# Kernel tuning notes

Measured on AMD Instinct MI355X. Metric: run time of the kernel, lower is better.

## Reference

```python
import jax, jax.numpy as jnp
import numpy as np

N = 16777216  # length of the returns series


def setup_inputs() -> dict:
    key = jax.random.key(0)
    returns = 0.01 * jax.random.normal(key, (N,), dtype=jnp.float32)
    return {
        "returns": returns,
        "omega": jnp.float32(0.01),
        "alpha": jnp.float32(0.1),
        "beta": jnp.float32(0.85),
    }


def reference(returns, omega, alpha, beta):
    # GARCH(1,1): h[0] = var(returns) (unbiased, matching torch.var default);
    # h[t] = omega + alpha * r[t-1]^2 + beta * h[t-1]
    h0 = jnp.var(returns, ddof=1)
    # drivers b_t = omega + alpha * r_{t-1}^2 for t = 1..n-1
    b = omega + alpha * jnp.square(returns[:-1])

    def step(h_prev, b_t):
        h_t = b_t + beta * h_prev
        return h_t, h_t

    _, h_rest = jax.lax.scan(step, h0, b)
    h = jnp.concatenate([h0[None], h_rest])  # [n]
    return jnp.sqrt(h), h
```

## Files before the change

### kernel.cpp

```cpp
#include <hip/hip_runtime.h>
#include <math.h>


#define KPW 2048
#define MAIN_BLOCK 256
#define FIX 256

typedef float v4f __attribute__((ext_vector_type(4)));

__global__ __launch_bounds__(MAIN_BLOCK, 8)
void garch_fused(const float* __restrict__ r, int n,
                 const float* __restrict__ pOmega, const float* __restrict__ pAlpha,
                 const float* __restrict__ pBeta,
                 float* __restrict__ out_sqrt, float* __restrict__ out_h,
                 double* __restrict__ partial) {
    const int lane = threadIdx.x & 63;
    const int wid  = threadIdx.x >> 6;
    const int gwave = (blockIdx.x * blockDim.x + threadIdx.x) >> 6;
    const int start = gwave * KPW;

    const float omega = *pOmega;
    const float alpha = *pAlpha;
    const float beta  = *pBeta;

    const float c1 = beta;
    const float c2 = c1 * c1;
    const float c3 = c2 * c1;
    const float c4 = c2 * c2;
    const float c8 = c4 * c4;
    const float c16 = c8 * c8;
    const float c32 = c16 * c16;
    const float c64 = c32 * c32;
    const float c128 = c64 * c64;

    double acc_s = 0.0, acc_q = 0.0;

    if (start + KPW <= n) {
        float pw1 = 1.0f;
        { float p = c1; int e = lane;
          if (e & 1)  pw1 *= p; p *= p;
          if (e & 2)  pw1 *= p; p *= p;
          if (e & 4)  pw1 *= p; p *= p;
          if (e & 8)  pw1 *= p; p *= p;
          if (e & 16) pw1 *= p; p *= p;
          if (e & 32) pw1 *= p; }
        float pw4 = 1.0f;
        { float p = c4; int e = lane;
          if (e & 1)  pw4 *= p; p *= p;
          if (e & 2)  pw4 *= p; p *= p;
          if (e & 4)  pw4 *= p; p *= p;
          if (e & 8)  pw4 *= p; p *= p;
          if (e & 16) pw4 *= p; p *= p;
          if (e & 32) pw4 *= p; }

        const float4* r4p = (const float4*)r;
        const int b4 = (start >> 2) + lane;

        float4 rv[8];
        #pragma unroll
        for (int k = 0; k < 8; ++k) rv[k] = r4p[b4 + 64 * k];

        float h_prev = 0.0f;
        float carry_r = 0.0f;
        if (start > 0) {
            float ra = r[start - 2 - lane];
            float rb = r[start - 66 - lane];
            carry_r  = r[start - 1];
            float ba = fmaf(alpha * ra, ra, omega);
            float bb = fmaf(alpha * rb, rb, omega);
            float part = pw1 * fmaf(c64, bb, ba);
            for (int d = 1; d < 64; d <<= 1) part += __shfl_xor(part, d, 64);
            h_prev = part;
        }

        #pragma unroll
        for (int k = 0; k < 8; k += 2) {
            float4 a = rv[k], b = rv[k + 1];
            float sf = ((a.x + a.y) + (a.z + a.w)) + ((b.x + b.y) + (b.z + b.w));
            float qf = fmaf(a.x, a.x, fmaf(a.y, a.y, fmaf(a.z, a.z, a.w * a.w)));
            qf = fmaf(b.x, b.x, fmaf(b.y, b.y, fmaf(b.z, b.z, fmaf(b.w, b.w, qf))));
            acc_s += (double)sf;
            acc_q += (double)qf;
        }

        #pragma unroll
        for (int k = 0; k < 8; ++k) {
            float4 v = rv[k];

            float prevw = __shfl_up(v.w, 1, 64);
            float segc  = (k == 0) ? carry_r : __shfl(rv[k - 1].w, 63, 64);
            float prev  = (lane == 0) ? segc : prevw;

            float b0 = fmaf(alpha * prev, prev, omega);
            float b1 = fmaf(alpha * v.x, v.x, omega);
            float b2 = fmaf(alpha * v.y, v.y, omega);
            float b3 = fmaf(alpha * v.z, v.z, omega);
            if (k == 0 && start == 0 && lane == 0) b0 = 0.0f;

            float B = fmaf(c1, b2, b3);
            B = fmaf(c2, b1, B);
            B = fmaf(c3, b0, B);

            float t;
            t = __shfl_up(B, 1, 64);  if (lane >= 1)  B = fmaf(c4,   t, B);
            t = __shfl_up(B, 2, 64);  if (lane >= 2)  B = fmaf(c8,   t, B);
            t = __shfl_up(B, 4, 64);  if (lane >= 4)  B = fmaf(c16,  t, B);
            t = __shfl_up(B, 8, 64);  if (lane >= 8)  B = fmaf(c32,  t, B);
            t = __shfl_up(B, 16, 64); if (lane >= 16) B = fmaf(c64,  t, B);
            t = __shfl_up(B, 32, 64); if (lane >= 32) B = fmaf(c128, t, B);

            float Bex = __shfl_up(B, 1, 64);
            if (lane == 0) Bex = 0.0f;
            float hb = fmaf(pw4, h_prev, Bex);

            float h0v = fmaf(c1, hb,  b0);
            float h1v = fmaf(c1, h0v, b1);
            float h2v = fmaf(c1, h1v, b2);
            float h3v = fmaf(c1, h2v, b3);

            v4f hs = {h0v, h1v, h2v, h3v};
            v4f sq = {sqrtf(h0v), sqrtf(h1v), sqrtf(h2v), sqrtf(h3v)};
            ((v4f*)out_h)[b4 + 64 * k]    = hs;
            ((v4f*)out_sqrt)[b4 + 64 * k] = sq;

            h_prev = __shfl(h3v, 63, 64);
        }
    } else if (start < n) {
        float h_prev = 0.0f;
        if (start > 0) {
            float pw1 = 1.0f;
            { float p = c1; int e = lane;
              if (e & 1)  pw1 *= p; p *= p;
              if (e & 2)  pw1 *= p; p *= p;
              if (e & 4)  pw1 *= p; p *= p;
              if (e & 8)  pw1 *= p; p *= p;
              if (e & 16) pw1 *= p; p *= p;
              if (e & 32) pw1 *= p; }
            float ra = r[start - 2 - lane];
            float rb = r[start - 66 - lane];
            float ba = fmaf(alpha * ra, ra, omega);
            float bb = fmaf(alpha * rb, rb, omega);
            float part = pw1 * fmaf(c64, bb, ba);
            for (int d = 1; d < 64; d <<= 1) part += __shfl_xor(part, d, 64);
            h_prev = part;
        }
        if (lane == 0) {
            float h = h_prev;
            float prevr = (start > 0) ? r[start - 1] : 0.0f;
            for (int tt = start; tt < n; ++tt) {
                float bb = fmaf(alpha * prevr, prevr, omega);
                if (tt == 0) bb = 0.0f;
                float hv = fmaf(beta, h, bb);
                out_sqrt[tt] = sqrtf(hv);
                out_h[tt] = hv;
                h = hv;
                prevr = r[tt];
                acc_s += (double)prevr;
                acc_q += (double)prevr * prevr;
            }
        }
    }

    for (int d = 1; d < 64; d <<= 1) {
        acc_s += __shfl_xor(acc_s, d, 64);
        acc_q += __shfl_xor(acc_q, d, 64);
    }
    __shared__ double ls[MAIN_BLOCK / 64], lq[MAIN_BLOCK / 64];
    if (lane == 0) { ls[wid] = acc_s; lq[wid] = acc_q; }
    __syncthreads();
    if (threadIdx.x == 0) {
        double S = 0.0, Q = 0.0;
        for (int w = 0; w < (int)(blockDim.x >> 6); ++w) { S += ls[w]; Q += lq[w]; }
        partial[2 * blockIdx.x]     = S;
        partial[2 * blockIdx.x + 1] = Q;
    }
}

__global__ void garch_finalize(const double* __restrict__ partial, int nblocks, int n,
                               const float* __restrict__ r,
                               const float* __restrict__ pOmega,
                               const float* __restrict__ pAlpha,
                               const float* __restrict__ pBeta,
                               float* __restrict__ out_sqrt, float* __restrict__ out_h) {
    __shared__ float rbuf[FIX];
    int fix = (n < FIX) ? n : FIX;
    for (int i = threadIdx.x; i < fix - 1; i += blockDim.x) rbuf[i] = r[i];

    double s = 0.0, q = 0.0;
    for (int i = threadIdx.x; i < nblocks; i += blockDim.x) {
        s += partial[2 * i];
        q += partial[2 * i + 1];
    }
    for (int d = 1; d < 64; d <<= 1) {
        s += __shfl_xor(s, d, 64);
        q += __shfl_xor(q, d, 64);
    }
    __shared__ double ls[4], lq[4];
    int wid = threadIdx.x >> 6, lane = threadIdx.x & 63;
    if (lane == 0) { ls[wid] = s; lq[wid] = q; }
    __syncthreads();
    if (threadIdx.x == 0) {
        double S = 0.0, Q = 0.0;
        for (int w = 0; w < (int)(blockDim.x >> 6); ++w) { S += ls[w]; Q += lq[w]; }
        double mean = S / (double)n;
        double var = (Q - (double)n * mean * mean) / (double)(n - 1);
        float h0 = (float)var;
        float omega = *pOmega, alpha = *pAlpha, beta = *pBeta;

        float h = h0;
        if (n > 0) { out_h[0] = h; out_sqrt[0] = sqrtf(h); }
        for (int t = 1; t < fix; ++t) {
            float rr = rbuf[t - 1];
            float b = fmaf(alpha * rr, rr, omega);
            h = fmaf(beta, h, b);
            out_h[t] = h;
            out_sqrt[t] = sqrtf(h);
        }
    }
}

extern "C" void kernel_launch(void* const* d_in, const int* in_sizes, int n_in,
                              void* d_out, int out_size, void* d_ws, size_t ws_size,
                              hipStream_t stream) {
    const float* r      = (const float*)d_in[0];
    const float* pOmega = (const float*)d_in[1];
    const float* pAlpha = (const float*)d_in[2];
    const float* pBeta  = (const float*)d_in[3];
    int n = in_sizes[0];

    float* out_sqrt = (float*)d_out;
    float* out_h    = out_sqrt + n;

    double* partial = (double*)d_ws;

    int elems_per_block = KPW * (MAIN_BLOCK / 64);
    int nblocks = (n + elems_per_block - 1) / elems_per_block;

    garch_fused<<<nblocks, MAIN_BLOCK, 0, stream>>>(
        r, n, pOmega, pAlpha, pBeta, out_sqrt, out_h, partial);
    garch_finalize<<<1, 256, 0, stream>>>(
        partial, nblocks, n, r, pOmega, pAlpha, pBeta, out_sqrt, out_h);
}
```

Before: 228.9 us.

## Double per-wave chunk and stream loads in a rolled loop instead of preloading

Each wave now processes 4096 elements instead of 2048, which halves the number of waves and the per-wave warm-up cost of the 128-element carry-in reduction. The 8-deep float4 preload with a fully unrolled scan is replaced by a rolled loop that loads one float4 per lane per 256-element step. A tail path handles partial chunks. The occupancy hint in launch bounds is dropped. In exchange, fewer loads are in flight per wave, each load now sits on the serial chain before its scan, and the grid has fewer blocks, so latency hiding may get worse.

```diff
diff --git a/kernel.cpp b/kernel.cpp
--- a/kernel.cpp
+++ b/kernel.cpp
@@ -2,13 +2,13 @@
 #include <math.h>
 
 
-#define KPW 2048
+#define KPW 4096
 #define MAIN_BLOCK 256
 #define FIX 256
 
 typedef float v4f __attribute__((ext_vector_type(4)));
 
-__global__ __launch_bounds__(MAIN_BLOCK, 8)
+__global__ __launch_bounds__(MAIN_BLOCK)
 void garch_fused(const float* __restrict__ r, int n,
                  const float* __restrict__ pOmega, const float* __restrict__ pAlpha,
                  const float* __restrict__ pBeta,
@@ -35,9 +35,9 @@
 
     double acc_s = 0.0, acc_q = 0.0;
 
-    if (start + KPW <= n) {
+    if (start < n) {
         float pw1 = 1.0f;
-        { float p = c1; int e = lane;
+        { float p = beta; int e = lane;
           if (e & 1)  pw1 *= p; p *= p;
           if (e & 2)  pw1 *= p; p *= p;
           if (e & 4)  pw1 *= p; p *= p;
@@ -53,89 +53,11 @@
           if (e & 16) pw4 *= p; p *= p;
           if (e & 32) pw4 *= p; }
 
-        const float4* r4p = (const float4*)r;
-        const int b4 = (start >> 2) + lane;
-
-        float4 rv[8];
-        #pragma unroll
-        for (int k = 0; k < 8; ++k) rv[k] = r4p[b4 + 64 * k];
-
-        float h_prev = 0.0f;
-        float carry_r = 0.0f;
-        if (start > 0) {
-            float ra = r[start - 2 - lane];
-            float rb = r[start - 66 - lane];
-            carry_r  = r[start - 1];
-            float ba = fmaf(alpha * ra, ra, omega);
-            float bb = fmaf(alpha * rb, rb, omega);
-            float part = pw1 * fmaf(c64, bb, ba);
-            for (int d = 1; d < 64; d <<= 1) part += __shfl_xor(part, d, 64);
-            h_prev = part;
-        }
-
-        #pragma unroll
-        for (int k = 0; k < 8; k += 2) {
-            float4 a = rv[k], b = rv[k + 1];
-            float sf = ((a.x + a.y) + (a.z + a.w)) + ((b.x + b.y) + (b.z + b.w));
-            float qf = fmaf(a.x, a.x, fmaf(a.y, a.y, fmaf(a.z, a.z, a.w * a.w)));
-            qf = fmaf(b.x, b.x, fmaf(b.y, b.y, fmaf(b.z, b.z, fmaf(b.w, b.w, qf))));
-            acc_s += (double)sf;
-            acc_q += (double)qf;
-        }
-
-        #pragma unroll
-        for (int k = 0; k < 8; ++k) {
-            float4 v = rv[k];
-
-            float prevw = __shfl_up(v.w, 1, 64);
-            float segc  = (k == 0) ? carry_r : __shfl(rv[k - 1].w, 63, 64);
-            float prev  = (lane == 0) ? segc : prevw;
-
-            float b0 = fmaf(alpha * prev, prev, omega);
-            float b1 = fmaf(alpha * v.x, v.x, omega);
-            float b2 = fmaf(alpha * v.y, v.y, omega);
-            float b3 = fmaf(alpha * v.z, v.z, omega);
-            if (k == 0 && start == 0 && lane == 0) b0 = 0.0f;
-
-            float B = fmaf(c1, b2, b3);
-            B = fmaf(c2, b1, B);
-            B = fmaf(c3, b0, B);
-
-            float t;
-            t = __shfl_up(B, 1, 64);  if (lane >= 1)  B = fmaf(c4,   t, B);
-            t = __shfl_up(B, 2, 64);  if (lane >= 2)  B = fmaf(c8,   t, B);
-            t = __shfl_up(B, 4, 64);  if (lane >= 4)  B = fmaf(c16,  t, B);
-            t = __shfl_up(B, 8, 64);  if (lane >= 8)  B = fmaf(c32,  t, B);
-            t = __shfl_up(B, 16, 64); if (lane >= 16) B = fmaf(c64,  t, B);
-            t = __shfl_up(B, 32, 64); if (lane >= 32) B = fmaf(c128, t, B);
-
-            float Bex = __shfl_up(B, 1, 64);
-            if (lane == 0) Bex = 0.0f;
-            float hb = fmaf(pw4, h_prev, Bex);
-
-            float h0v = fmaf(c1, hb,  b0);
-            float h1v = fmaf(c1, h0v, b1);
-            float h2v = fmaf(c1, h1v, b2);
-            float h3v = fmaf(c1, h2v, b3);
-
-            v4f hs = {h0v, h1v, h2v, h3v};
-            v4f sq = {sqrtf(h0v), sqrtf(h1v), sqrtf(h2v), sqrtf(h3v)};
-            ((v4f*)out_h)[b4 + 64 * k]    = hs;
-            ((v4f*)out_sqrt)[b4 + 64 * k] = sq;
-
-            h_prev = __shfl(h3v, 63, 64);
-        }
-    } else if (start < n) {
-        float h_prev = 0.0f;
-        if (start > 0) {
-            float pw1 = 1.0f;
-            { float p = c1; int e = lane;
-              if (e & 1)  pw1 *= p; p *= p;
-              if (e & 2)  pw1 *= p; p *= p;
-              if (e & 4)  pw1 *= p; p *= p;
-              if (e & 8)  pw1 *= p; p *= p;
-              if (e & 16) pw1 *= p; p *= p;
-              if (e & 32) pw1 *= p; }
+        float h_prev, r_carry;
+        if (start == 0) {
+            h_prev = 0.0f;
+            r_carry = 0.0f;
+        } else {
             float ra = r[start - 2 - lane];
             float rb = r[start - 66 - lane];
             float ba = fmaf(alpha * ra, ra, omega);
@@ -143,11 +65,67 @@
             float part = pw1 * fmaf(c64, bb, ba);
             for (int d = 1; d < 64; d <<= 1) part += __shfl_xor(part, d, 64);
             h_prev = part;
-        }
-        if (lane == 0) {
+            r_carry = r[start - 1];
+        }
+
+        int end = start + KPW; if (end > n) end = n;
+        const float4* r4p = (const float4*)r;
+
+        int s = start;
+        for (; s + 256 <= end; s += 256) {
+            float4 rv = r4p[(s >> 2) + lane];
+
+            float sf = (rv.x + rv.y) + (rv.z + rv.w);
+            float qf = fmaf(rv.x, rv.x,
+                       fmaf(rv.y, rv.y,
+                       fmaf(rv.z, rv.z, rv.w * rv.w)));
+            acc_s += (double)sf;
+            acc_q += (double)qf;
+
+            float prev = __shfl_up(rv.w, 1, 64);
+            if (lane == 0) prev = r_carry;
+
+            float b0 = fmaf(alpha * prev, prev, omega);
+            float b1 = fmaf(alpha * rv.x, rv.x, omega);
+            float b2 = fmaf(alpha * rv.y, rv.y, omega);
+            float b3 = fmaf(alpha * rv.z, rv.z, omega);
+            if (s == 0 && lane == 0) b0 = 0.0f;
+
+            float B = fmaf(c1, b2, b3);
+            B = fmaf(c2, b1, B);
+            B = fmaf(c3, b0, B);
+
+            float t;
+            t = __shfl_up(B, 1, 64);  if (lane >= 1)  B = fmaf(c4,  t, B);
+            t = __shfl_up(B, 2, 64);  if (lane >= 2)  B = fmaf(c8,  t, B);
+            t = __shfl_up(B, 4, 64);  if (lane >= 4)  B = fmaf(c16, t, B);
+            t = __shfl_up(B, 8, 64);  if (lane >= 8)  B = fmaf(c32, t, B);
+            t = __shfl_up(B, 16, 64); if (lane >= 16) B = fmaf(c64, t, B);
+            t = __shfl_up(B, 32, 64); if (lane >= 32) B = fmaf(c128, t, B);
+
+            float Bex = __shfl_up(B, 1, 64);
+            if (lane == 0) Bex = 0.0f;
+            float h_base = fmaf(pw4, h_prev, Bex);
+
+            float h0v = fmaf(c1, h_base, b0);
+            float h1v = fmaf(c1, h0v, b1);
+            float h2v = fmaf(c1, h1v, b2);
+            float h3v = fmaf(c1, h2v, b3);
+
+            int idx4 = (s >> 2) + lane;
+            v4f hs = {h0v, h1v, h2v, h3v};
+            v4f sq = {sqrtf(h0v), sqrtf(h1v), sqrtf(h2v), sqrtf(h3v)};
+            ((v4f*)out_sqrt)[idx4] = sq;
+            ((v4f*)out_h)[idx4]    = hs;
+
+            h_prev  = __shfl(h3v, 63, 64);
+            r_carry = __shfl(rv.w, 63, 64);
+        }
+
+        if (s < end && lane == 0) {
             float h = h_prev;
-            float prevr = (start > 0) ? r[start - 1] : 0.0f;
-            for (int tt = start; tt < n; ++tt) {
+            float prevr = r_carry;
+            for (int tt = s; tt < end; ++tt) {
                 float bb = fmaf(alpha * prevr, prevr, omega);
                 if (tt == 0) bb = 0.0f;
                 float hv = fmaf(beta, h, bb);
```

After: 208.4 us. 8.9% less time.
